# Optimization experiments

Hardware: AMD Instinct MI355X
Metric: run time of the kernel (lower is better)

## Reference

```python
import jax, jax.numpy as jnp
import numpy as np

SQRT2 = 1.41421356237
BASE_SCALE = 0.001
CDF_X = 10.0


def erf_poly(x):
    # Abramowitz-Stegun polynomial erf, exactly as the torch source
    sign = jnp.where(x > 0, 1.0, -1.0)  # torch: (x > 0) * 2 - 1
    x = jnp.abs(x)
    a1, a2, a3, a4, a5 = 0.254829592, -0.284496736, 1.421413741, -1.453152027, 1.061405429
    p = 0.3275911
    t = 1.0 / (1.0 + p * x)
    y = 1.0 - ((((a5 * t + a4) * t + a3) * t + a2) * t + a1) * t * jnp.exp(-x * x)
    return sign * y


def rot6d_to_rotmat(x):
    # Zhou et al. 6D rotation: Gram-Schmidt two columns, cross for third
    a1, a2 = x[..., :3], x[..., 3:6]
    b1 = a1 / jnp.linalg.norm(a1, axis=-1, keepdims=True)
    b2 = a2 - jnp.sum(b1 * a2, axis=-1, keepdims=True) * b1
    b2 = b2 / jnp.linalg.norm(b2, axis=-1, keepdims=True)
    b3 = jnp.cross(b1, b2)
    return jnp.stack([b1, b2, b3], axis=-1)  # columns b1,b2,b3 -> [..., 3, 3]


def setup_inputs() -> dict:
    key = jax.random.key(0)
    k1, k2, k3, k4 = jax.random.split(key, 4)
    R, B, G = 65536, 24, 4
    return {
        "w2ls": jax.random.normal(k1, (R, B, 4, 4), dtype=jnp.float32),
        "rays_o": jax.random.normal(k2, (R, 3), dtype=jnp.float32),
        "rays_d": jax.random.normal(k3, (R, 3), dtype=jnp.float32),
        "Gs": jax.random.normal(k4, (B, G, 13), dtype=jnp.float32),
        "N_unique": 1,
    }


def reference(w2ls, rays_o, rays_d, Gs, N_unique):
    # Gs-derived quantities are detached in the original get_1D_gaussians
    Gs = jax.lax.stop_gradient(Gs)
    R = rays_o.shape[0]
    dt = rays_o.dtype

    origins = jnp.concatenate([rays_o, jnp.ones((R, 1), dt)], axis=1)      # [r,4]
    dirs = jnp.concatenate([rays_d, jnp.zeros((R, 1), dt)], axis=1)        # [r,4]
    o = jnp.einsum('rbij,rj->rbi', w2ls, origins)[..., :3]                 # [r,b,3]
    n = jnp.einsum('rbij,rj->rbi', w2ls, dirs)[..., :3]                    # [r,b,3]

    G_mu = Gs[..., 0:3]                                                    # [b,g,3]
    G_std = jnp.abs(Gs[..., 3:6]) + BASE_SCALE                             # [b,g,3]
    G_R = rot6d_to_rotmat(Gs[..., 6:12])                                   # [b,g,3,3]
    G_c = jnp.abs(Gs[..., 12])                                             # [b,g]

    # S = diag(1/std); SR = S @ R scales rows of R
    SR = G_R / G_std[..., None]                                            # [b,g,3,3]
    Sn1 = jnp.einsum('bgki,bgkj->bgij', SR, SR)                            # R^T S^2 R

    mu_d_o = G_mu[None] - o[:, :, None, :]                                 # [r,b,g,3]
    nSn = jnp.einsum('rbi,bgij,rbj->rbg', n, Sn1, n)                       # n^T Sn1 n
    sigma_bar_sqr = 1.0 / nSn                                              # [r,b,g]
    mu_bar = jnp.einsum('rbi,bgij,rbgj->rbg', n, Sn1, mu_d_o) * sigma_bar_sqr
    quad = jnp.einsum('rbgi,bgij,rbgj->rbg', mu_d_o, Sn1, mu_d_o)

    densities = G_c[None] * jnp.exp(-0.5 * (quad - mu_bar ** 2 / sigma_bar_sqr))
    means = mu_bar
    sigmas = jnp.sqrt(sigma_bar_sqr)

    # soft density filter (weights computed on detached means)
    w = jax.nn.sigmoid(100.0 * jax.lax.stop_gradient(means) - 1.0)
    densities = densities * w

    # gaussian1d_cdf at x = 10.0, then shadow map: sum over all (bone, gaussian)
    cdf = densities * 0.5 * (1.0 + erf_poly((CDF_X - means) / (sigmas * SQRT2)))
    shadow_map = jnp.exp(-jnp.sum(cdf, axis=(1, 2)))                       # [r]
    return shadow_map
```

## Files before the change

### kernel.cpp

```cpp
#include <hip/hip_runtime.h>
#include <math.h>


#define NB 24
#define NG 4
#define BASE_SCALE 0.001f

template <int CTRL>
__device__ __forceinline__ float dpp_f(float x) {
    int r = __builtin_amdgcn_update_dpp(0, __float_as_int(x), CTRL, 0xF, 0xF, true);
    return __int_as_float(r);
}

__device__ __forceinline__ float frcp(float x) { return __builtin_amdgcn_rcpf(x); }
__device__ __forceinline__ float fexp2(float x) { return __builtin_amdgcn_exp2f(x); }

__global__ __launch_bounds__(256, 8) void gauss_vis_kernel(
    const float* __restrict__ w2ls,
    const float* __restrict__ rays_o,
    const float* __restrict__ rays_d,
    const float* __restrict__ Gs,
    float* __restrict__ out,
    int R)
{
    __shared__ float4 P[NB * NG * 3];

    const int tid = threadIdx.x;
    const int gid = blockIdx.x * 256 + tid;
    const int ray0 = gid >> 3;
    const int ray = ray0 < R ? ray0 : (R - 1);
    const int oct = tid & 7;
    const int sub = oct & 3;
    const int half = oct >> 2;

    if (tid < NB * NG) {
        const float* gp = Gs + tid * 13;
        float mu0 = gp[0], mu1 = gp[1], mu2 = gp[2];
        float s0 = fabsf(gp[3]) + BASE_SCALE;
        float s1 = fabsf(gp[4]) + BASE_SCALE;
        float s2 = fabsf(gp[5]) + BASE_SCALE;
        float ax = gp[6], ay = gp[7], az = gp[8];
        float bx = gp[9], by = gp[10], bz = gp[11];
        float c = fabsf(gp[12]);
        float inv1 = 1.0f / sqrtf(ax * ax + ay * ay + az * az);
        float b1x = ax * inv1, b1y = ay * inv1, b1z = az * inv1;
        float dot = b1x * bx + b1y * by + b1z * bz;
        float t2x = bx - dot * b1x, t2y = by - dot * b1y, t2z = bz - dot * b1z;
        float inv2 = 1.0f / sqrtf(t2x * t2x + t2y * t2y + t2z * t2z);
        float b2x = t2x * inv2, b2y = t2y * inv2, b2z = t2z * inv2;
        float b3x = b1y * b2z - b1z * b2y;
        float b3y = b1z * b2x - b1x * b2z;
        float b3z = b1x * b2y - b1y * b2x;
        float w0 = 1.0f / (s0 * s0), w1 = 1.0f / (s1 * s1), w2 = 1.0f / (s2 * s2);
        float s00 = b1x * b1x * w0 + b1y * b1y * w1 + b1z * b1z * w2;
        float s01 = b1x * b2x * w0 + b1y * b2y * w1 + b1z * b2z * w2;
        float s02 = b1x * b3x * w0 + b1y * b3y * w1 + b1z * b3z * w2;
        float s11 = b2x * b2x * w0 + b2y * b2y * w1 + b2z * b2z * w2;
        float s12 = b2x * b3x * w0 + b2y * b3y * w1 + b2z * b3z * w2;
        float s22 = b3x * b3x * w0 + b3y * b3y * w1 + b3z * b3z * w2;
        float u00 = sqrtf(fmaxf(s00, 1e-20f));
        float iu00 = 1.0f / u00;
        float u01 = s01 * iu00;
        float u02 = s02 * iu00;
        float u11 = sqrtf(fmaxf(s11 - u01 * u01, 1e-20f));
        float u12 = (s12 - u01 * u02) / u11;
        float u22 = sqrtf(fmaxf(s22 - u02 * u02 - u12 * u12, 1e-20f));
        P[tid * 3 + 0] = make_float4(u00, u01, u02, u11);
        P[tid * 3 + 1] = make_float4(u12, u22, mu0, mu1);
        P[tid * 3 + 2] = make_float4(mu2, c, 0.f, 0.f);
    }
    __syncthreads();

    const float rox = rays_o[ray * 3 + 0];
    const float roy = rays_o[ray * 3 + 1];
    const float roz = rays_o[ray * 3 + 2];
    const float rdx = rays_d[ray * 3 + 0];
    const float rdy = rays_d[ray * 3 + 1];
    const float rdz = rays_d[ray * 3 + 2];

    const float4* __restrict__ Wp =
        (const float4*)w2ls + ((size_t)ray * (NB * 4) + half * 4 + sub);
    const int pi0 = (half * NG + sub) * 3;

    float sum = 0.f;
#pragma unroll 2
    for (int k = 0; k < 12; ++k) {
        const float4 M = Wp[k * 8];
        float o_s = fmaf(M.x, rox, fmaf(M.y, roy, fmaf(M.z, roz, M.w)));
        float n_s = fmaf(M.x, rdx, fmaf(M.y, rdy, M.z * rdz));
        float o0 = dpp_f<0x00>(o_s), o1 = dpp_f<0x55>(o_s), o2 = dpp_f<0xAA>(o_s);
        float n0 = dpp_f<0x00>(n_s), n1 = dpp_f<0x55>(n_s), n2 = dpp_f<0xAA>(n_s);

        int pi = pi0 + k * 24;
        float4 p0 = P[pi + 0];
        float4 p1 = P[pi + 1];
        float4 p2 = P[pi + 2];
        float u00 = p0.x, u01 = p0.y, u02 = p0.z, u11 = p0.w;
        float u12 = p1.x, u22 = p1.y;
        float d0 = p1.z - o0, d1 = p1.w - o1, d2 = p2.x - o2;
        float c = p2.y;

        float un0 = fmaf(u02, n2, fmaf(u01, n1, u00 * n0));
        float un1 = fmaf(u12, n2, u11 * n1);
        float un2 = u22 * n2;
        float ud0 = fmaf(u02, d2, fmaf(u01, d1, u00 * d0));
        float ud1 = fmaf(u12, d2, u11 * d1);
        float ud2 = u22 * d2;

        float nSn = fmaf(un2, un2, fmaf(un1, un1, un0 * un0));
        float nSd = fmaf(un2, ud2, fmaf(un1, ud1, un0 * ud0));
        float quad = fmaf(ud2, ud2, fmaf(ud1, ud1, ud0 * ud0));

        float r = __builtin_amdgcn_rsqf(nSn);
        float t = nSd * r;
        float resid = fmaf(t, t, -quad);

        float ed = fexp2(0.72134752f * resid);
        float ew = fexp2(fmaf(t * r, -144.26950f, 1.4426950f));
        float z = r * fmaf(nSn, 10.f, -nSd);
        float zz = z * z;
        float ec = fexp2(-z * fmaf(0.10180843f, zz, 2.3048389f));

        float denom = (1.f + ew) * (1.f + ec);
        sum = fmaf(c * ed, frcp(denom), sum);
    }

    sum += dpp_f<0xB1>(sum);
    sum += dpp_f<0x4E>(sum);
    sum += __shfl_xor(sum, 4, 64);
    if (oct == 0 && ray0 < R) out[ray0] = __expf(-sum);
}

extern "C" void kernel_launch(void* const* d_in, const int* in_sizes, int n_in,
                              void* d_out, int out_size, void* d_ws, size_t ws_size,
                              hipStream_t stream) {
    const float* w2ls   = (const float*)d_in[0];
    const float* rays_o = (const float*)d_in[1];
    const float* rays_d = (const float*)d_in[2];
    const float* Gs     = (const float*)d_in[3];
    float* out = (float*)d_out;

    const int R = in_sizes[1] / 3;
    const int threads = 256;
    const long long total = (long long)R * 8;
    const int blocks = (int)((total + threads - 1) / threads);
    gauss_vis_kernel<<<blocks, threads, 0, stream>>>(w2ls, rays_o, rays_d, Gs, out, R);
}
```

Baseline: 22.45 us.

## Pack two bones per lane into float2 vectors and fold log amplitude into exponent

Gaussian parameters are repacked in shared memory so that each lane processes bones k and k+12 together as float2 pairs. The math then runs through packed FMA (v_pk_fma_f32) and the loop becomes 6 iterations with two w2ls loads each. The amplitude is stored as log2(c) and added inside the exp2 argument, which removes a multiply. This is meant to roughly halve the VALU instruction count, at the cost of a more complex LDS layout and more register pressure. If c is zero, log2 gives -inf, which still produces zero.

Result: no change. 22.25 us, median of 2 (-0.9%).

```diff
diff --git a/kernel.cpp b/kernel.cpp
--- a/kernel.cpp
+++ b/kernel.cpp
@@ -5,6 +5,9 @@
 #define NB 24
 #define NG 4
 #define BASE_SCALE 0.001f
+
+typedef float f2 __attribute__((ext_vector_type(2)));
+#define PKF(a, b, c) __builtin_elementwise_fma((f2)(a), (f2)(b), (f2)(c))
 
 template <int CTRL>
 __device__ __forceinline__ float dpp_f(float x) {
@@ -23,7 +26,7 @@
     float* __restrict__ out,
     int R)
 {
-    __shared__ float4 P[NB * NG * 3];
+    __shared__ float4 Ppk4[6 * 2 * 4 * 5];
 
     const int tid = threadIdx.x;
     const int gid = blockIdx.x * 256 + tid;
@@ -34,6 +37,7 @@
     const int half = oct >> 2;
 
     if (tid < NB * NG) {
+        const int b = tid >> 2, g = tid & 3;
         const float* gp = Gs + tid * 13;
         float mu0 = gp[0], mu1 = gp[1], mu2 = gp[2];
         float s0 = fabsf(gp[3]) + BASE_SCALE;
@@ -65,9 +69,16 @@
         float u11 = sqrtf(fmaxf(s11 - u01 * u01, 1e-20f));
         float u12 = (s12 - u01 * u02) / u11;
         float u22 = sqrtf(fmaxf(s22 - u02 * u02 - u12 * u12, 1e-20f));
-        P[tid * 3 + 0] = make_float4(u00, u01, u02, u11);
-        P[tid * 3 + 1] = make_float4(u12, u22, mu0, mu1);
-        P[tid * 3 + 2] = make_float4(mu2, c, 0.f, 0.f);
+        float lc = log2f(c);
+        const int sel = b >= 12 ? 1 : 0;
+        const int bb = b - 12 * sel;
+        const int j = bb >> 1, hlf = b & 1;
+        float* dst = (float*)&Ppk4[((j * 2 + hlf) * 4 + g) * 5];
+        dst[0 * 2 + sel] = u00;  dst[1 * 2 + sel] = u01;
+        dst[2 * 2 + sel] = u02;  dst[3 * 2 + sel] = u11;
+        dst[4 * 2 + sel] = u12;  dst[5 * 2 + sel] = u22;
+        dst[6 * 2 + sel] = mu0;  dst[7 * 2 + sel] = mu1;
+        dst[8 * 2 + sel] = mu2;  dst[9 * 2 + sel] = lc;
     }
     __syncthreads();
 
@@ -79,51 +90,72 @@
     const float rdz = rays_d[ray * 3 + 2];
 
     const float4* __restrict__ Wp =
-        (const float4*)w2ls + ((size_t)ray * (NB * 4) + half * 4 + sub);
-    const int pi0 = (half * NG + sub) * 3;
+        (const float4*)w2ls + ((size_t)ray * 96 + half * 4 + sub);
+    const float4* __restrict__ Pb = Ppk4 + (half * 4 + sub) * 5;
 
-    float sum = 0.f;
-#pragma unroll 2
-    for (int k = 0; k < 12; ++k) {
-        const float4 M = Wp[k * 8];
-        float o_s = fmaf(M.x, rox, fmaf(M.y, roy, fmaf(M.z, roz, M.w)));
-        float n_s = fmaf(M.x, rdx, fmaf(M.y, rdy, M.z * rdz));
-        float o0 = dpp_f<0x00>(o_s), o1 = dpp_f<0x55>(o_s), o2 = dpp_f<0xAA>(o_s);
-        float n0 = dpp_f<0x00>(n_s), n1 = dpp_f<0x55>(n_s), n2 = dpp_f<0xAA>(n_s);
+    const f2 C_ED  = {0.72134752f, 0.72134752f};
+    const f2 C_EWm = {-144.26950f, -144.26950f};
+    const f2 C_EWb = {1.4426950f, 1.4426950f};
+    const f2 C_ECa = {0.10180843f, 0.10180843f};
+    const f2 C_ECb = {2.3048389f, 2.3048389f};
+    const f2 C_ONE = {1.f, 1.f};
+    const f2 C_TEN = {10.f, 10.f};
 
-        int pi = pi0 + k * 24;
-        float4 p0 = P[pi + 0];
-        float4 p1 = P[pi + 1];
-        float4 p2 = P[pi + 2];
-        float u00 = p0.x, u01 = p0.y, u02 = p0.z, u11 = p0.w;
-        float u12 = p1.x, u22 = p1.y;
-        float d0 = p1.z - o0, d1 = p1.w - o1, d2 = p2.x - o2;
-        float c = p2.y;
+    f2 sum2 = {0.f, 0.f};
+#pragma unroll 1
+    for (int j = 0; j < 6; ++j) {
+        const float4 MA = Wp[j * 8];
+        const float4 MB = Wp[j * 8 + 48];
+        float o_sA = fmaf(MA.x, rox, fmaf(MA.y, roy, fmaf(MA.z, roz, MA.w)));
+        float o_sB = fmaf(MB.x, rox, fmaf(MB.y, roy, fmaf(MB.z, roz, MB.w)));
+        float n_sA = fmaf(MA.x, rdx, fmaf(MA.y, rdy, MA.z * rdz));
+        float n_sB = fmaf(MB.x, rdx, fmaf(MB.y, rdy, MB.z * rdz));
+        f2 o0, o1, o2, n0, n1, n2;
+        o0.x = dpp_f<0x00>(o_sA); o0.y = dpp_f<0x00>(o_sB);
+        o1.x = dpp_f<0x55>(o_sA); o1.y = dpp_f<0x55>(o_sB);
+        o2.x = dpp_f<0xAA>(o_sA); o2.y = dpp_f<0xAA>(o_sB);
+        n0.x = dpp_f<0x00>(n_sA); n0.y = dpp_f<0x00>(n_sB);
+        n1.x = dpp_f<0x55>(n_sA); n1.y = dpp_f<0x55>(n_sB);
+        n2.x = dpp_f<0xAA>(n_sA); n2.y = dpp_f<0xAA>(n_sB);
 
-        float un0 = fmaf(u02, n2, fmaf(u01, n1, u00 * n0));
-        float un1 = fmaf(u12, n2, u11 * n1);
-        float un2 = u22 * n2;
-        float ud0 = fmaf(u02, d2, fmaf(u01, d1, u00 * d0));
-        float ud1 = fmaf(u12, d2, u11 * d1);
-        float ud2 = u22 * d2;
+        const float4* pp = Pb + j * 40;
+        float4 q0 = pp[0], q1 = pp[1], q2 = pp[2], q3 = pp[3], q4 = pp[4];
+        f2 u00 = ((const f2*)&q0)[0], u01 = ((const f2*)&q0)[1];
+        f2 u02 = ((const f2*)&q1)[0], u11 = ((const f2*)&q1)[1];
+        f2 u12 = ((const f2*)&q2)[0], u22 = ((const f2*)&q2)[1];
+        f2 mu0 = ((const f2*)&q3)[0], mu1 = ((const f2*)&q3)[1];
+        f2 mu2 = ((const f2*)&q4)[0], lc  = ((const f2*)&q4)[1];
 
-        float nSn = fmaf(un2, un2, fmaf(un1, un1, un0 * un0));
-        float nSd = fmaf(un2, ud2, fmaf(un1, ud1, un0 * ud0));
-        float quad = fmaf(ud2, ud2, fmaf(ud1, ud1, ud0 * ud0));
+        f2 d0 = mu0 - o0, d1 = mu1 - o1, d2 = mu2 - o2;
+        f2 un0 = PKF(u02, n2, PKF(u01, n1, u00 * n0));
+        f2 un1 = PKF(u12, n2, u11 * n1);
+        f2 un2 = u22 * n2;
+        f2 ud0 = PKF(u02, d2, PKF(u01, d1, u00 * d0));
+        f2 ud1 = PKF(u12, d2, u11 * d1);
+        f2 ud2 = u22 * d2;
+        f2 nSn = PKF(un2, un2, PKF(un1, un1, un0 * un0));
+        f2 nSd = PKF(un2, ud2, PKF(un1, ud1, un0 * ud0));
+        f2 quad = PKF(ud2, ud2, PKF(ud1, ud1, ud0 * ud0));
 
-        float r = __builtin_amdgcn_rsqf(nSn);
-        float t = nSd * r;
-        float resid = fmaf(t, t, -quad);
-
-        float ed = fexp2(0.72134752f * resid);
-        float ew = fexp2(fmaf(t * r, -144.26950f, 1.4426950f));
-        float z = r * fmaf(nSn, 10.f, -nSd);
-        float zz = z * z;
-        float ec = fexp2(-z * fmaf(0.10180843f, zz, 2.3048389f));
-
-        float denom = (1.f + ew) * (1.f + ec);
-        sum = fmaf(c * ed, frcp(denom), sum);
+        f2 r; r.x = __builtin_amdgcn_rsqf(nSn.x); r.y = __builtin_amdgcn_rsqf(nSn.y);
+        f2 t = nSd * r;
+        f2 resid = PKF(t, t, -quad);
+        f2 mean = t * r;
+        f2 edarg = PKF(C_ED, resid, lc);
+        f2 ewarg = PKF(mean, C_EWm, C_EWb);
+        f2 zi = PKF(nSn, C_TEN, -nSd);
+        f2 z = zi * r;
+        f2 zz = z * z;
+        f2 ecarg = -z * PKF(C_ECa, zz, C_ECb);
+        f2 ed, ew, ec;
+        ed.x = fexp2(edarg.x); ed.y = fexp2(edarg.y);
+        ew.x = fexp2(ewarg.x); ew.y = fexp2(ewarg.y);
+        ec.x = fexp2(ecarg.x); ec.y = fexp2(ecarg.y);
+        f2 den = (C_ONE + ew) * (C_ONE + ec);
+        f2 rd; rd.x = frcp(den.x); rd.y = frcp(den.y);
+        sum2 = PKF(ed, rd, sum2);
     }
+    float sum = sum2.x + sum2.y;
 
     sum += dpp_f<0xB1>(sum);
     sum += dpp_f<0x4E>(sum);
```
